# Performance work log

Hardware: AMD Instinct MI355X
Metric: run time of the kernel (lower is better)

Reference implementation:

```python
import jax, jax.numpy as jnp
import numpy as np

B, S, D, H = 4, 2048, 1024, 16
HD = D // H  # 64


def apply_rotary(x, cos, sin):
    # x: (b, h, s, hd); cos/sin: (s, hd)
    x1, x2 = x[..., : HD // 2], x[..., HD // 2 :]
    rotated = jnp.concatenate((-x2, x1), axis=-1)
    return x * cos + rotated * sin


def setup_inputs() -> dict:
    key = jax.random.key(0)
    ks = jax.random.split(key, 12)
    x = jax.random.normal(ks[0], (B, S, D), dtype=jnp.float32)
    # RoPE tables
    inv_freq = 1.0 / (10000.0 ** (jnp.arange(0, HD, 2, dtype=jnp.float32) / HD))
    t = jnp.arange(S, dtype=jnp.float32)
    freqs = jnp.outer(t, inv_freq)            # (S, HD/2)
    emb = jnp.concatenate((freqs, freqs), -1)  # (S, HD)
    cos, sin = jnp.cos(emb), jnp.sin(emb)
    # causal additive mask
    neg = jnp.finfo(jnp.float32).min
    attn_mask = jnp.where(jnp.tril(jnp.ones((S, S), dtype=bool)), 0.0, neg)[None, None]
    sc = 1.0 / np.sqrt(D)
    Wq = jax.random.normal(ks[1], (D, D), jnp.float32) * sc
    bq = jnp.zeros((D,), jnp.float32)
    Wk = jax.random.normal(ks[2], (D, D), jnp.float32) * sc
    bk = jnp.zeros((D,), jnp.float32)
    Wv = jax.random.normal(ks[3], (D, D), jnp.float32) * sc
    bv = jnp.zeros((D,), jnp.float32)
    Wo = jax.random.normal(ks[4], (D, D), jnp.float32) * sc
    bo = jnp.zeros((D,), jnp.float32)
    return {"x": x, "cos": cos, "sin": sin, "attn_mask": attn_mask,
            "Wq": Wq, "bq": bq, "Wk": Wk, "bk": bk, "Wv": Wv, "bv": bv,
            "Wo": Wo, "bo": bo}


def reference(x, cos, sin, attn_mask, Wq, bq, Wk, bk, Wv, bv, Wo, bo):
    b, s, d = x.shape
    scale = HD ** -0.5
    def proj(W, bias):
        return (x @ W.T + bias).reshape(b, s, H, HD).transpose(0, 2, 1, 3)
    q = apply_rotary(proj(Wq, bq), cos, sin)
    k = apply_rotary(proj(Wk, bk), cos, sin)
    v = proj(Wv, bv)
    scores = jnp.einsum("bhqd,bhkd->bhqk", q, k) * scale + attn_mask
    w = jax.nn.softmax(scores, axis=-1)  # dropout is identity in eval / p=0
    out = jnp.einsum("bhqk,bhkd->bhqd", w, v)
    out = out.transpose(0, 2, 1, 3).reshape(b, s, d)
    return out @ Wo.T + bo
```

## Files before the change

### kernel.cpp

```cpp
#include <hip/hip_runtime.h>

#define Bc 4
#define Sc 2048
#define Dc 1024
#define Hc 16
#define HDc 64
#define Mrows (Bc * Sc)

typedef __bf16 bf16x8 __attribute__((ext_vector_type(8)));
typedef float f32x4 __attribute__((ext_vector_type(4)));

#define FIX2 23.0831207f
#define QSCALE 0.18033688f

__device__ __forceinline__ unsigned short f2b(float f) {
  unsigned int u = __builtin_bit_cast(unsigned int, f);
  u += 0x7fffu + ((u >> 16) & 1u);
  return (unsigned short)(u >> 16);
}

__device__ __forceinline__ unsigned int pack2(float lo, float hi) {
  return (unsigned int)f2b(lo) | ((unsigned int)f2b(hi) << 16);
}

__device__ __forceinline__ unsigned int pack2t(float lo, float hi) {
  return __builtin_amdgcn_perm(__builtin_bit_cast(unsigned int, hi),
                               __builtin_bit_cast(unsigned int, lo), 0x07060302u);
}

__device__ __forceinline__ float fexp2(float x) {
#if __has_builtin(__builtin_amdgcn_exp2f)
  return __builtin_amdgcn_exp2f(x);
#else
  return exp2f(x);
#endif
}

__device__ __forceinline__ bf16x8 ld8(const unsigned short* p) {
  return __builtin_bit_cast(bf16x8, *(const uint4*)p);
}

__device__ __forceinline__ f32x4 mfma16(bf16x8 a, bf16x8 b, f32x4 c) {
  return __builtin_amdgcn_mfma_f32_16x16x32_bf16(a, b, c, 0, 0, 0);
}

__device__ __forceinline__ void async16(const unsigned short* g, unsigned short* l) {
  __builtin_amdgcn_global_load_lds(
      (const __attribute__((address_space(1))) unsigned int*)g,
      (__attribute__((address_space(3))) unsigned int*)l, 16, 0, 0);
}

__global__ __launch_bounds__(256) void cast_all(const float* __restrict__ x,
                                                const float* __restrict__ w0,
                                                const float* __restrict__ w1,
                                                const float* __restrict__ w2,
                                                const float* __restrict__ w3,
                                                unsigned short* __restrict__ xo,
                                                unsigned short* __restrict__ o0,
                                                unsigned short* __restrict__ o1,
                                                unsigned short* __restrict__ o2,
                                                unsigned short* __restrict__ o3) {
  int blk = blockIdx.x;
  const float* src;
  unsigned short* dst;
  if (blk < 8192) {
    src = x; dst = xo;
  } else {
    const int which = (blk - 8192) >> 10;
    src = which == 0 ? w0 : which == 1 ? w1 : which == 2 ? w2 : w3;
    dst = which == 0 ? o0 : which == 1 ? o1 : which == 2 ? o2 : o3;
    blk = (blk - 8192) & 1023;
  }
  const int i = (blk * 256 + threadIdx.x) * 4;
  float4 f = *(const float4*)(src + i);
  ushort4 o;
  o.x = f2b(f.x); o.y = f2b(f.y); o.z = f2b(f.z); o.w = f2b(f.w);
  *(ushort4*)(dst + i) = o;
}

__global__ __launch_bounds__(256) void gemm_qkv(const unsigned short* __restrict__ A,
                                                const unsigned short* __restrict__ Wqp,
                                                const unsigned short* __restrict__ Wkp,
                                                const unsigned short* __restrict__ Wvp,
                                                const float* __restrict__ bqp,
                                                const float* __restrict__ bkp,
                                                const float* __restrict__ bvp,
                                                unsigned short* __restrict__ Qo,
                                                unsigned short* __restrict__ Ko,
                                                unsigned short* __restrict__ Vto,
                                                const float* __restrict__ cosT,
                                                const float* __restrict__ sinT) {
  constexpr int K = Dc;
  __shared__ __align__(16) unsigned short As[128 * 64];
  __shared__ __align__(16) unsigned short Bs[128 * 64];

  const int which = blockIdx.x >> 3;
  const int nb = (blockIdx.x & 7) * 128;
  const unsigned short* W = which == 0 ? Wqp : which == 1 ? Wkp : Wvp;
  const float* bias = which == 0 ? bqp : which == 1 ? bkp : bvp;
  const int mb = blockIdx.y * 128;
  const int t = threadIdx.x;
  const int lane = t & 63;
  const int quad = lane >> 4, l16 = lane & 15;
  const int wm = (t >> 6) >> 1, wn = (t >> 6) & 1;

  f32x4 acc[4][4] = {};

  const int srow = t >> 3;
  const int schunk = (t & 7) ^ (srow & 7);
  const unsigned short* gA = A + (size_t)(mb + srow) * K + schunk * 8;
  const unsigned short* gW = W + (size_t)(nb + srow) * K + schunk * 8;
  const int ldsOff = t * 8;

  for (int k0 = 0; k0 < K; k0 += 64) {
    __syncthreads();
#pragma unroll
    for (int o = 0; o < 4; ++o) {
      async16(gA + (size_t)o * 32 * K + k0, &As[ldsOff + o * 2048]);
      async16(gW + (size_t)o * 32 * K + k0, &Bs[ldsOff + o * 2048]);
    }
    __syncthreads();

#pragma unroll
    for (int kk = 0; kk < 2; ++kk) {
      bf16x8 af[4], bf[4];
#pragma unroll
      for (int i = 0; i < 4; ++i) {
        const int ar = wm * 64 + i * 16 + l16;
        af[i] = ld8(&As[ar * 64 + ((kk * 4 + quad) ^ (ar & 7)) * 8]);
        const int br = wn * 64 + i * 16 + l16;
        bf[i] = ld8(&Bs[br * 64 + ((kk * 4 + quad) ^ (br & 7)) * 8]);
      }
#pragma unroll
      for (int i = 0; i < 4; ++i)
#pragma unroll
        for (int j = 0; j < 4; ++j)
          acc[i][j] = mfma16(af[i], bf[j], acc[i][j]);
    }
  }

  float bn[4];
#pragma unroll
  for (int j = 0; j < 4; ++j) bn[j] = bias[nb + wn * 64 + j * 16 + l16];

  if (which < 2) {
    unsigned short* out = which == 0 ? Qo : Ko;
    const float sc = which == 0 ? QSCALE : 1.0f;
#pragma unroll
    for (int i = 0; i < 4; ++i)
#pragma unroll
      for (int r = 0; r < 4; ++r) {
        const int m = mb + wm * 64 + i * 16 + quad * 4 + r;
        const int s = m & (Sc - 1);
        float v[4];
#pragma unroll
        for (int j = 0; j < 4; ++j) v[j] = acc[i][j][r] + bn[j];
#pragma unroll
        for (int j = 0; j < 4; ++j) {
          const int hd = j * 16 + l16;
          const float c = cosT[s * HDc + hd];
          const float sn = sinT[s * HDc + hd];
          float o = (j < 2) ? (v[j] * c - v[j ^ 2] * sn)
                            : (v[j] * c + v[j ^ 2] * sn);
          out[(size_t)m * Dc + nb + wn * 64 + hd] = f2b(o * sc);
        }
      }
  } else {
#pragma unroll
    for (int i = 0; i < 4; ++i)
#pragma unroll
      for (int r = 0; r < 4; ++r) {
        const int m = mb + wm * 64 + i * 16 + quad * 4 + r;
        const int s = m & (Sc - 1);
        const int b = m >> 11;
#pragma unroll
        for (int j = 0; j < 4; ++j) {
          const int n = nb + wn * 64 + j * 16 + l16;
          const int h = n >> 6, hd = n & 63;
          Vto[(size_t)((b * Hc + h) * HDc + hd) * Sc + s] = f2b(acc[i][j][r] + bn[j]);
        }
      }
  }
}

__global__ __launch_bounds__(256) void gemm_out(const unsigned short* __restrict__ A,
                                                const unsigned short* __restrict__ W,
                                                const float* __restrict__ bias,
                                                float* __restrict__ out) {
  constexpr int N = Dc, K = Dc;
  __shared__ __align__(16) unsigned short As[128 * 64];
  __shared__ __align__(16) unsigned short Bs[128 * 64];

  const int nb = blockIdx.x * 128;
  const int mb = blockIdx.y * 128;
  const int t = threadIdx.x;
  const int lane = t & 63;
  const int quad = lane >> 4, l16 = lane & 15;
  const int wm = (t >> 6) >> 1, wn = (t >> 6) & 1;

  f32x4 acc[4][4] = {};

  const int srow = t >> 3;
  const int schunk = (t & 7) ^ (srow & 7);
  const unsigned short* gA = A + (size_t)(mb + srow) * K + schunk * 8;
  const unsigned short* gW = W + (size_t)(nb + srow) * K + schunk * 8;
  const int ldsOff = t * 8;

  for (int k0 = 0; k0 < K; k0 += 64) {
    __syncthreads();
#pragma unroll
    for (int o = 0; o < 4; ++o) {
      async16(gA + (size_t)o * 32 * K + k0, &As[ldsOff + o * 2048]);
      async16(gW + (size_t)o * 32 * K + k0, &Bs[ldsOff + o * 2048]);
    }
    __syncthreads();

#pragma unroll
    for (int kk = 0; kk < 2; ++kk) {
      bf16x8 af[4], bf[4];
#pragma unroll
      for (int i = 0; i < 4; ++i) {
        const int ar = wm * 64 + i * 16 + l16;
        af[i] = ld8(&As[ar * 64 + ((kk * 4 + quad) ^ (ar & 7)) * 8]);
        const int br = wn * 64 + i * 16 + l16;
        bf[i] = ld8(&Bs[br * 64 + ((kk * 4 + quad) ^ (br & 7)) * 8]);
      }
#pragma unroll
      for (int i = 0; i < 4; ++i)
#pragma unroll
        for (int j = 0; j < 4; ++j)
          acc[i][j] = mfma16(af[i], bf[j], acc[i][j]);
    }
  }

  float bn[4];
#pragma unroll
  for (int j = 0; j < 4; ++j) bn[j] = bias[nb + wn * 64 + j * 16 + l16];
#pragma unroll
  for (int i = 0; i < 4; ++i)
#pragma unroll
    for (int r = 0; r < 4; ++r) {
      const int m = mb + wm * 64 + i * 16 + quad * 4 + r;
#pragma unroll
      for (int j = 0; j < 4; ++j)
        out[(size_t)m * N + nb + wn * 64 + j * 16 + l16] = acc[i][j][r] + bn[j];
    }
}

__global__ __launch_bounds__(256) void attn_kernel(const unsigned short* __restrict__ Q,
                                                   const unsigned short* __restrict__ K,
                                                   const unsigned short* __restrict__ Vt,
                                                   unsigned short* __restrict__ O) {
  __shared__ __align__(16) unsigned short Ks[2][64 * 64];
  __shared__ __align__(16) unsigned short Vs[2][64 * 64];

  const int bh = blockIdx.x;
  const int b = bh >> 4, h = bh & 15;
  const int wave = threadIdx.x >> 6, lane = threadIdx.x & 63;
  const int quad = lane >> 4, l16 = lane & 15;

  int kSrc[2], vSrc[2], sDst[2];
#pragma unroll
  for (int o = 0; o < 2; ++o) {
    const int R = wave * 16 + o * 8 + (lane >> 3);
    const int slot = lane & 7;
    const int rr = R & 31;
    const int key = (R >> 5) * 32 + ((rr >> 2) & 3) * 8 + ((rr >> 4) & 1) * 4 + (rr & 3);
    const int chunk = slot ^ (R & 7);
    kSrc[o] = key * Dc + chunk * 8;
    vSrc[o] = R * Sc + chunk * 8;
    sDst[o] = wave * 1024 + o * 512 + lane * 8;
  }
  const unsigned short* kBase = K + (size_t)b * Sc * Dc + h * HDc;
  const unsigned short* vBase = Vt + (size_t)(b * Hc + h) * HDc * Sc;

  auto stage = [&](int buf, int kb) {
#pragma unroll
    for (int o = 0; o < 2; ++o) {
      async16(kBase + (size_t)kb * Dc + kSrc[o], &Ks[buf][sDst[o]]);
      async16(vBase + kb + vSrc[o], &Vs[buf][sDst[o]]);
    }
  };

#pragma unroll 1
  for (int sidx = 0; sidx < 2; ++sidx) {
    const int qt = sidx == 0 ? (int)blockIdx.y : 15 - (int)blockIdx.y;
    const int qbase = qt * 128;
    const int wbase = qbase + wave * 32;
    const int wave_max_q = wbase + 31;
    const int nkt = 2 * qt + 2;

    bf16x8 qf[2][2];
#pragma unroll
    for (int mt = 0; mt < 2; ++mt) {
      const unsigned short* qp =
          Q + (size_t)(b * Sc + wbase + mt * 16 + l16) * Dc + h * HDc + quad * 8;
      qf[mt][0] = ld8(qp);
      qf[mt][1] = ld8(qp + 32);
    }

    float lsum[2] = {0.f, 0.f};
    f32x4 accO[2][4] = {};

    __syncthreads();
    stage(0, 0);
    for (int t = 0; t < nkt; ++t) {
      __syncthreads();
      if (t + 1 < nkt) stage((t + 1) & 1, (t + 1) * 64);
      const int kb = t * 64;
      if (kb > wave_max_q) continue;
      const unsigned short* KsB = &Ks[t & 1][0];
      const unsigned short* VsB = &Vs[t & 1][0];

#pragma unroll
      for (int c = 0; c < 2; ++c) {
        const int kc = kb + c * 32;
        if (kc > wave_max_q) break;
        const bool partial = (kc + 31 > wbase);

        bf16x8 kf[2][2], vf[4];
#pragma unroll
        for (int tt = 0; tt < 2; ++tt) {
          const int row = c * 32 + tt * 16 + l16;
#pragma unroll
          for (int kk = 0; kk < 2; ++kk)
            kf[tt][kk] = ld8(&KsB[row * 64 + (((kk * 4 + quad) ^ (l16 & 7)) * 8)]);
        }
#pragma unroll
        for (int ct = 0; ct < 4; ++ct)
          vf[ct] = ld8(&VsB[(ct * 16 + l16) * 64 + (((c * 4 + quad) ^ (l16 & 7)) * 8)]);

#pragma unroll
        for (int mt = 0; mt < 2; ++mt) {
          f32x4 st[2];
#pragma unroll
          for (int tt = 0; tt < 2; ++tt) {
            st[tt] = mfma16(kf[tt][0], qf[mt][0], f32x4{-FIX2, -FIX2, -FIX2, -FIX2});
            st[tt] = mfma16(kf[tt][1], qf[mt][1], st[tt]);
          }
          const int q = wbase + mt * 16 + l16;
          unsigned int w[4];
          float ls = 0.f;
#pragma unroll
          for (int tt = 0; tt < 2; ++tt)
#pragma unroll
            for (int rp = 0; rp < 2; ++rp) {
              const int key0 = kc + quad * 8 + tt * 4 + 2 * rp;
              float s0 = st[tt][2 * rp], s1 = st[tt][2 * rp + 1];
              if (partial) {
                s0 = (key0     <= q) ? s0 : -1e30f;
                s1 = (key0 + 1 <= q) ? s1 : -1e30f;
              }
              const float p0 = fexp2(s0);
              const float p1 = fexp2(s1);
              ls += p0 + p1;
              w[tt * 2 + rp] = pack2t(p0, p1);
            }
          lsum[mt] += ls;
          const bf16x8 pB = __builtin_bit_cast(bf16x8, uint4{w[0], w[1], w[2], w[3]});
#pragma unroll
          for (int ct = 0; ct < 4; ++ct)
            accO[mt][ct] = mfma16(vf[ct], pB, accO[mt][ct]);
        }
      }
    }

#pragma unroll
    for (int mt = 0; mt < 2; ++mt) {
      float l = lsum[mt];
      l += __shfl_xor(l, 16);
      l += __shfl_xor(l, 32);
      const float inv = 1.f / l;
      const int m = wbase + mt * 16 + l16;
      unsigned short* op = O + (size_t)(b * Sc + m) * Dc + h * HDc;
#pragma unroll
      for (int ct = 0; ct < 4; ++ct) {
        const unsigned int lo = pack2(accO[mt][ct][0] * inv, accO[mt][ct][1] * inv);
        const unsigned int hi = pack2(accO[mt][ct][2] * inv, accO[mt][ct][3] * inv);
        *(uint2*)(op + ct * 16 + quad * 4) = uint2{lo, hi};
      }
    }
  }
}

extern "C" void kernel_launch(void* const* d_in, const int* in_sizes, int n_in,
                              void* d_out, int out_size, void* d_ws, size_t ws_size,
                              hipStream_t stream) {
  const float* x = (const float*)d_in[0];
  const float* cosT = (const float*)d_in[1];
  const float* sinT = (const float*)d_in[2];
  const float* Wq = (const float*)d_in[4];
  const float* bq = (const float*)d_in[5];
  const float* Wk = (const float*)d_in[6];
  const float* bk = (const float*)d_in[7];
  const float* Wv = (const float*)d_in[8];
  const float* bv = (const float*)d_in[9];
  const float* Wo = (const float*)d_in[10];
  const float* bo = (const float*)d_in[11];

  char* p = (char*)d_ws;
  auto alloc = [&](size_t bytes) { char* r = p; p += bytes; return r; };
  const size_t XB = (size_t)Mrows * Dc * 2;
  const size_t WB = (size_t)Dc * Dc * 2;
  unsigned short* xb  = (unsigned short*)alloc(XB);
  unsigned short* wqb = (unsigned short*)alloc(WB);
  unsigned short* wkb = (unsigned short*)alloc(WB);
  unsigned short* wvb = (unsigned short*)alloc(WB);
  unsigned short* wob = (unsigned short*)alloc(WB);
  unsigned short* Qb  = (unsigned short*)alloc(XB);
  unsigned short* Kb  = (unsigned short*)alloc(XB);
  unsigned short* Vtb = (unsigned short*)alloc(XB);
  unsigned short* Ob  = (unsigned short*)alloc(XB);

  cast_all<<<12288, 256, 0, stream>>>(x, Wq, Wk, Wv, Wo, xb, wqb, wkb, wvb, wob);

  gemm_qkv<<<dim3(24, Mrows / 128), 256, 0, stream>>>(
      xb, wqb, wkb, wvb, bq, bk, bv, Qb, Kb, Vtb, cosT, sinT);

  attn_kernel<<<dim3(Bc * Hc, 8), 256, 0, stream>>>(Qb, Kb, Vtb, Ob);

  gemm_out<<<dim3(Dc / 128, Mrows / 128), 256, 0, stream>>>(Ob, wob, bo, (float*)d_out);
}
```

Before: 270.5 us.

## Store Q/K/V in MFMA-fragment order and load attention operands directly from global

The QKV GEMM epilogue now writes Q, K and V per head in a layout matching the MFMA fragment each lane needs, so a lane's 8 bf16 values are contiguous. The attention kernel drops its LDS double-buffered K/V staging and barriers, and each wave reads its fragments directly with 16-byte global loads. The grid changes from 8 blocks handling paired causal tiles to 16 blocks each handling one query tile. This removes LDS traffic and block-wide synchronisation, but the four waves in a block now each fetch K/V from global/L2, and the paired-tile load balancing is lost.

```diff
diff --git a/kernel.cpp b/kernel.cpp
--- a/kernel.cpp
+++ b/kernel.cpp
@@ -6,6 +6,7 @@
 #define Hc 16
 #define HDc 64
 #define Mrows (Bc * Sc)
+#define HEADSZ (Sc * HDc)
 
 typedef __bf16 bf16x8 __attribute__((ext_vector_type(8)));
 typedef float f32x4 __attribute__((ext_vector_type(4)));
@@ -85,9 +86,9 @@
                                                 const float* __restrict__ bqp,
                                                 const float* __restrict__ bkp,
                                                 const float* __restrict__ bvp,
-                                                unsigned short* __restrict__ Qo,
-                                                unsigned short* __restrict__ Ko,
-                                                unsigned short* __restrict__ Vto,
+                                                unsigned short* __restrict__ Qp,
+                                                unsigned short* __restrict__ Kp,
+                                                unsigned short* __restrict__ Vp,
                                                 const float* __restrict__ cosT,
                                                 const float* __restrict__ sinT) {
   constexpr int K = Dc;
@@ -143,8 +144,10 @@
 #pragma unroll
   for (int j = 0; j < 4; ++j) bn[j] = bias[nb + wn * 64 + j * 16 + l16];
 
+  const int h = (nb + wn * 64) >> 6;
+
   if (which < 2) {
-    unsigned short* out = which == 0 ? Qo : Ko;
+    unsigned short* out = which == 0 ? Qp : Kp;
     const float sc = which == 0 ? QSCALE : 1.0f;
 #pragma unroll
     for (int i = 0; i < 4; ++i)
@@ -152,6 +155,8 @@
       for (int r = 0; r < 4; ++r) {
         const int m = mb + wm * 64 + i * 16 + quad * 4 + r;
         const int s = m & (Sc - 1);
+        const int b = m >> 11;
+        const size_t head = ((size_t)b * Hc + h) * HEADSZ;
         float v[4];
 #pragma unroll
         for (int j = 0; j < 4; ++j) v[j] = acc[i][j][r] + bn[j];
@@ -162,7 +167,17 @@
           const float sn = sinT[s * HDc + hd];
           float o = (j < 2) ? (v[j] * c - v[j ^ 2] * sn)
                             : (v[j] * c + v[j ^ 2] * sn);
-          out[(size_t)m * Dc + nb + wn * 64 + hd] = f2b(o * sc);
+          const int kk = hd >> 5, qd = (hd >> 3) & 3, jj = hd & 7;
+          size_t f;
+          if (which == 0) {
+            f = (size_t)(((s >> 4) * 2 + kk) * 512) + (s & 15) * 32 + qd * 8 + jj;
+          } else {
+            const int g = s >> 5, kl = s & 31;
+            const int tt = (kl >> 2) & 1;
+            const int l16k = ((kl >> 3) << 2) | (kl & 3);
+            f = (size_t)((((g * 2 + kk) * 2 + tt) * 512)) + l16k * 32 + qd * 8 + jj;
+          }
+          out[head + f] = f2b(o * sc);
         }
       }
   } else {
@@ -173,11 +188,13 @@
         const int m = mb + wm * 64 + i * 16 + quad * 4 + r;
         const int s = m & (Sc - 1);
         const int b = m >> 11;
+        const size_t head = ((size_t)b * Hc + h) * HEADSZ;
+        const int g = s >> 5, kl = s & 31;
+        const int qv = kl >> 3, jv = kl & 7;
 #pragma unroll
         for (int j = 0; j < 4; ++j) {
-          const int n = nb + wn * 64 + j * 16 + l16;
-          const int h = n >> 6, hd = n & 63;
-          Vto[(size_t)((b * Hc + h) * HDc + hd) * Sc + s] = f2b(acc[i][j][r] + bn[j]);
+          Vp[head + (size_t)(((g * 4 + j) * 16 + l16) * 32) + qv * 8 + jv] =
+              f2b(acc[i][j][r] + bn[j]);
         }
       }
   }
@@ -247,138 +264,96 @@
     }
 }
 
-__global__ __launch_bounds__(256) void attn_kernel(const unsigned short* __restrict__ Q,
-                                                   const unsigned short* __restrict__ K,
+__global__ __launch_bounds__(256) void attn_kernel(const unsigned short* __restrict__ Qp,
+                                                   const unsigned short* __restrict__ Kp,
                                                    const unsigned short* __restrict__ Vt,
                                                    unsigned short* __restrict__ O) {
-  __shared__ __align__(16) unsigned short Ks[2][64 * 64];
-  __shared__ __align__(16) unsigned short Vs[2][64 * 64];
-
   const int bh = blockIdx.x;
+  const int qt = 15 - (int)blockIdx.y;
   const int b = bh >> 4, h = bh & 15;
   const int wave = threadIdx.x >> 6, lane = threadIdx.x & 63;
   const int quad = lane >> 4, l16 = lane & 15;
-
-  int kSrc[2], vSrc[2], sDst[2];
-#pragma unroll
-  for (int o = 0; o < 2; ++o) {
-    const int R = wave * 16 + o * 8 + (lane >> 3);
-    const int slot = lane & 7;
-    const int rr = R & 31;
-    const int key = (R >> 5) * 32 + ((rr >> 2) & 3) * 8 + ((rr >> 4) & 1) * 4 + (rr & 3);
-    const int chunk = slot ^ (R & 7);
-    kSrc[o] = key * Dc + chunk * 8;
-    vSrc[o] = R * Sc + chunk * 8;
-    sDst[o] = wave * 1024 + o * 512 + lane * 8;
-  }
-  const unsigned short* kBase = K + (size_t)b * Sc * Dc + h * HDc;
-  const unsigned short* vBase = Vt + (size_t)(b * Hc + h) * HDc * Sc;
-
-  auto stage = [&](int buf, int kb) {
-#pragma unroll
-    for (int o = 0; o < 2; ++o) {
-      async16(kBase + (size_t)kb * Dc + kSrc[o], &Ks[buf][sDst[o]]);
-      async16(vBase + kb + vSrc[o], &Vs[buf][sDst[o]]);
-    }
-  };
-
-#pragma unroll 1
-  for (int sidx = 0; sidx < 2; ++sidx) {
-    const int qt = sidx == 0 ? (int)blockIdx.y : 15 - (int)blockIdx.y;
-    const int qbase = qt * 128;
-    const int wbase = qbase + wave * 32;
-    const int wave_max_q = wbase + 31;
-    const int nkt = 2 * qt + 2;
-
-    bf16x8 qf[2][2];
+  const int laneOff = (l16 * 4 + quad) * 8;
+
+  const size_t head = (size_t)bh * HEADSZ;
+  const unsigned short* Kh = Kp + head + laneOff;
+  const unsigned short* Vh = Vt + head + laneOff;
+
+  const int wbase = qt * 128 + wave * 32;
+  const int qg = wbase >> 4;
+
+  bf16x8 qf[2][2];
+#pragma unroll
+  for (int mt = 0; mt < 2; ++mt)
+#pragma unroll
+    for (int kk = 0; kk < 2; ++kk)
+      qf[mt][kk] = ld8(Qp + head + (size_t)(((qg + mt) * 2 + kk) * 512) + laneOff);
+
+  float lsum[2] = {0.f, 0.f};
+  f32x4 accO[2][4] = {};
+
+  const int ng = (wbase >> 5) + 1;
+  for (int gi = 0; gi < ng; ++gi) {
+    const int kc = gi * 32;
+    const bool partial = (kc + 31 > wbase);
+
+    bf16x8 kf[2][2], vf[4];
+#pragma unroll
+    for (int tt = 0; tt < 2; ++tt)
+#pragma unroll
+      for (int kk = 0; kk < 2; ++kk)
+        kf[tt][kk] = ld8(Kh + (size_t)(((gi * 2 + kk) * 2 + tt) * 512));
+#pragma unroll
+    for (int ct = 0; ct < 4; ++ct)
+      vf[ct] = ld8(Vh + (size_t)((gi * 4 + ct) * 512));
+
 #pragma unroll
     for (int mt = 0; mt < 2; ++mt) {
-      const unsigned short* qp =
-          Q + (size_t)(b * Sc + wbase + mt * 16 + l16) * Dc + h * HDc + quad * 8;
-      qf[mt][0] = ld8(qp);
-      qf[mt][1] = ld8(qp + 32);
-    }
-
-    float lsum[2] = {0.f, 0.f};
-    f32x4 accO[2][4] = {};
-
-    __syncthreads();
-    stage(0, 0);
-    for (int t = 0; t < nkt; ++t) {
-      __syncthreads();
-      if (t + 1 < nkt) stage((t + 1) & 1, (t + 1) * 64);
-      const int kb = t * 64;
-      if (kb > wave_max_q) continue;
-      const unsigned short* KsB = &Ks[t & 1][0];
-      const unsigned short* VsB = &Vs[t & 1][0];
-
-#pragma unroll
-      for (int c = 0; c < 2; ++c) {
-        const int kc = kb + c * 32;
-        if (kc > wave_max_q) break;
-        const bool partial = (kc + 31 > wbase);
-
-        bf16x8 kf[2][2], vf[4];
-#pragma unroll
-        for (int tt = 0; tt < 2; ++tt) {
-          const int row = c * 32 + tt * 16 + l16;
-#pragma unroll
-          for (int kk = 0; kk < 2; ++kk)
-            kf[tt][kk] = ld8(&KsB[row * 64 + (((kk * 4 + quad) ^ (l16 & 7)) * 8)]);
+      f32x4 st[2];
+#pragma unroll
+      for (int tt = 0; tt < 2; ++tt) {
+        st[tt] = mfma16(kf[tt][0], qf[mt][0], f32x4{-FIX2, -FIX2, -FIX2, -FIX2});
+        st[tt] = mfma16(kf[tt][1], qf[mt][1], st[tt]);
+      }
+      const int q = wbase + mt * 16 + l16;
+      unsigned int w[4];
+      float ls = 0.f;
+#pragma unroll
+      for (int tt = 0; tt < 2; ++tt)
+#pragma unroll
+        for (int rp = 0; rp < 2; ++rp) {
+          const int key0 = kc + quad * 8 + tt * 4 + 2 * rp;
+          float s0 = st[tt][2 * rp], s1 = st[tt][2 * rp + 1];
+          if (partial) {
+            s0 = (key0     <= q) ? s0 : -1e30f;
+            s1 = (key0 + 1 <= q) ? s1 : -1e30f;
+          }
+          const float p0 = fexp2(s0);
+          const float p1 = fexp2(s1);
+          ls += p0 + p1;
+          w[tt * 2 + rp] = pack2t(p0, p1);
         }
-#pragma unroll
-        for (int ct = 0; ct < 4; ++ct)
-          vf[ct] = ld8(&VsB[(ct * 16 + l16) * 64 + (((c * 4 + quad) ^ (l16 & 7)) * 8)]);
-
-#pragma unroll
-        for (int mt = 0; mt < 2; ++mt) {
-          f32x4 st[2];
-#pragma unroll
-          for (int tt = 0; tt < 2; ++tt) {
-            st[tt] = mfma16(kf[tt][0], qf[mt][0], f32x4{-FIX2, -FIX2, -FIX2, -FIX2});
-            st[tt] = mfma16(kf[tt][1], qf[mt][1], st[tt]);
-          }
-          const int q = wbase + mt * 16 + l16;
-          unsigned int w[4];
-          float ls = 0.f;
-#pragma unroll
-          for (int tt = 0; tt < 2; ++tt)
-#pragma unroll
-            for (int rp = 0; rp < 2; ++rp) {
-              const int key0 = kc + quad * 8 + tt * 4 + 2 * rp;
-              float s0 = st[tt][2 * rp], s1 = st[tt][2 * rp + 1];
-              if (partial) {
-                s0 = (key0     <= q) ? s0 : -1e30f;
-                s1 = (key0 + 1 <= q) ? s1 : -1e30f;
-              }
-              const float p0 = fexp2(s0);
-              const float p1 = fexp2(s1);
-              ls += p0 + p1;
-              w[tt * 2 + rp] = pack2t(p0, p1);
-            }
-          lsum[mt] += ls;
-          const bf16x8 pB = __builtin_bit_cast(bf16x8, uint4{w[0], w[1], w[2], w[3]});
-#pragma unroll
-          for (int ct = 0; ct < 4; ++ct)
-            accO[mt][ct] = mfma16(vf[ct], pB, accO[mt][ct]);
-        }
-      }
-    }
-
-#pragma unroll
-    for (int mt = 0; mt < 2; ++mt) {
-      float l = lsum[mt];
-      l += __shfl_xor(l, 16);
-      l += __shfl_xor(l, 32);
-      const float inv = 1.f / l;
-      const int m = wbase + mt * 16 + l16;
-      unsigned short* op = O + (size_t)(b * Sc + m) * Dc + h * HDc;
-#pragma unroll
-      for (int ct = 0; ct < 4; ++ct) {
-        const unsigned int lo = pack2(accO[mt][ct][0] * inv, accO[mt][ct][1] * inv);
-        const unsigned int hi = pack2(accO[mt][ct][2] * inv, accO[mt][ct][3] * inv);
-        *(uint2*)(op + ct * 16 + quad * 4) = uint2{lo, hi};
-      }
+      lsum[mt] += ls;
+      const bf16x8 pB = __builtin_bit_cast(bf16x8, uint4{w[0], w[1], w[2], w[3]});
+#pragma unroll
+      for (int ct = 0; ct < 4; ++ct)
+        accO[mt][ct] = mfma16(vf[ct], pB, accO[mt][ct]);
+    }
+  }
+
+#pragma unroll
+  for (int mt = 0; mt < 2; ++mt) {
+    float l = lsum[mt];
+    l += __shfl_xor(l, 16);
+    l += __shfl_xor(l, 32);
+    const float inv = 1.f / l;
+    const int m = wbase + mt * 16 + l16;
+    unsigned short* op = O + (size_t)(b * Sc + m) * Dc + h * HDc;
+#pragma unroll
+    for (int ct = 0; ct < 4; ++ct) {
+      const unsigned int lo = pack2(accO[mt][ct][0] * inv, accO[mt][ct][1] * inv);
+      const unsigned int hi = pack2(accO[mt][ct][2] * inv, accO[mt][ct][3] * inv);
+      *(uint2*)(op + ct * 16 + quad * 4) = uint2{lo, hi};
     }
   }
 }
@@ -407,17 +382,17 @@
   unsigned short* wkb = (unsigned short*)alloc(WB);
   unsigned short* wvb = (unsigned short*)alloc(WB);
   unsigned short* wob = (unsigned short*)alloc(WB);
-  unsigned short* Qb  = (unsigned short*)alloc(XB);
-  unsigned short* Kb  = (unsigned short*)alloc(XB);
-  unsigned short* Vtb = (unsigned short*)alloc(XB);
+  unsigned short* Qp  = (unsigned short*)alloc(XB);
+  unsigned short* Kp  = (unsigned short*)alloc(XB);
+  unsigned short* Vp  = (unsigned short*)alloc(XB);
   unsigned short* Ob  = (unsigned short*)alloc(XB);
 
   cast_all<<<12288, 256, 0, stream>>>(x, Wq, Wk, Wv, Wo, xb, wqb, wkb, wvb, wob);
 
   gemm_qkv<<<dim3(24, Mrows / 128), 256, 0, stream>>>(
-      xb, wqb, wkb, wvb, bq, bk, bv, Qb, Kb, Vtb, cosT, sinT);
-
-  attn_kernel<<<dim3(Bc * Hc, 8), 256, 0, stream>>>(Qb, Kb, Vtb, Ob);
+      xb, wqb, wkb, wvb, bq, bk, bv, Qp, Kp, Vp, cosT, sinT);
+
+  attn_kernel<<<dim3(Bc * Hc, 16), 256, 0, stream>>>(Qp, Kp, Vp, Ob);
 
   gemm_out<<<dim3(Dc / 128, Mrows / 128), 256, 0, stream>>>(Ob, wob, bo, (float*)d_out);
 }
```

After: 308.8 us. 14.2% more time.
